# Optimization experiments

Measured on AMD Instinct MI355X. Metric: run time of the kernel, lower is better.

## Reference

```python
import jax, jax.numpy as jnp
import numpy as np

V, D, NH, L, T, B = 32000, 768, 12, 4, 2048, 1
HD = D // NH
THETA = 10000.0
EPS = 1e-5


def setup_inputs() -> dict:
    key = jax.random.key(0)
    ks = jax.random.split(key, 12)
    s = 0.02
    return {
        "idx": jax.random.randint(ks[0], (B, T), 0, V),
        "wte": jax.random.normal(ks[1], (V, D), jnp.float32) * s,
        "ln1_w": jnp.ones((L, D), jnp.float32),
        "attn_w": jax.random.normal(ks[2], (L, 3 * D, D), jnp.float32) * s,
        "attnproj_w": jax.random.normal(ks[3], (L, D, D), jnp.float32) * s,
        "ln2_w": jnp.ones((L, D), jnp.float32),
        "fc_w": jax.random.normal(ks[4], (L, 4 * D, D), jnp.float32) * s,
        "fc_b": jnp.zeros((L, 4 * D), jnp.float32),
        "proj_w": jax.random.normal(ks[5], (L, D, 4 * D), jnp.float32) * s,
        "proj_b": jnp.zeros((L, D), jnp.float32),
        "lnf_w": jnp.ones((D,), jnp.float32),
        "unemb_b": jnp.zeros((V,), jnp.float32),
    }


def _ln(x, w):
    mu = jnp.mean(x, axis=-1, keepdims=True)
    var = jnp.mean(jnp.square(x - mu), axis=-1, keepdims=True)
    return (x - mu) * jax.lax.rsqrt(var + EPS) * w


def _rope(x, cos, sin):
    # x: [B,NH,T,HD]; cos/sin: [T,HD//2]
    x1, x2 = x[..., : HD // 2], x[..., HD // 2 :]
    return jnp.concatenate([x1 * cos - x2 * sin, x1 * sin + x2 * cos], axis=-1)


def _forward(idx, wte, ln1_w, attn_w, attnproj_w, ln2_w, fc_w, fc_b, proj_w, proj_b, lnf_w, unemb_b):
    x = wte[idx]  # [B,T,D]
    inv_freq = 1.0 / (THETA ** (jnp.arange(0, HD, 2, dtype=jnp.float32) / HD))  # [HD/2]
    t = jnp.arange(T, dtype=jnp.float32)
    freqs = jnp.outer(t, inv_freq)  # [T, HD/2]
    cos, sin = jnp.cos(freqs), jnp.sin(freqs)
    causal = jnp.tril(jnp.ones((T, T), bool))
    scale = 1.0 / jnp.sqrt(jnp.asarray(HD, x.dtype))
    for l in range(L):
        h = _ln(x, ln1_w[l])
        qkv = h @ attn_w[l].T  # [B,T,3D]
        q, k, v = jnp.split(qkv, 3, axis=-1)
        q = q.reshape(B, T, NH, HD).transpose(0, 2, 1, 3)
        k = k.reshape(B, T, NH, HD).transpose(0, 2, 1, 3)
        v = v.reshape(B, T, NH, HD).transpose(0, 2, 1, 3)
        q, k = _rope(q, cos, sin), _rope(k, cos, sin)
        att = jnp.einsum("bhqd,bhkd->bhqk", q, k) * scale
        att = jnp.where(causal, att, -jnp.inf)
        att = jax.nn.softmax(att, axis=-1)
        y = jnp.einsum("bhqk,bhkd->bhqd", att, v)
        y = y.transpose(0, 2, 1, 3).reshape(B, T, D)
        x = x + y @ attnproj_w[l].T
        h = _ln(x, ln2_w[l])
        m = jax.nn.gelu(h @ fc_w[l].T + fc_b[l], approximate=False)
        x = x + m @ proj_w[l].T + proj_b[l]
    x = _ln(x, lnf_w)
    return x @ wte.T + unemb_b  # tied unembedding, [B,T,V]


def reference(idx, wte, ln1_w, attn_w, attnproj_w, ln2_w, fc_w, fc_b, proj_w, proj_b, lnf_w, unemb_b):
    return _forward(idx, wte, ln1_w, attn_w, attnproj_w, ln2_w, fc_w, fc_b, proj_w, proj_b, lnf_w, unemb_b)
```

## Files before the change

### kernel.cpp

```cpp
#include <hip/hip_runtime.h>
#include <hip/hip_bf16.h>

typedef __bf16 bf16_t;
typedef __bf16 bf16x8 __attribute__((ext_vector_type(8)));
typedef __bf16 bf16x4 __attribute__((ext_vector_type(4)));
typedef float  f32x4  __attribute__((ext_vector_type(4)));

__device__ __forceinline__ void gl_lds16(const void* g, void* l) {
    __builtin_amdgcn_global_load_lds(
        (__attribute__((address_space(1))) void*)g,
        (__attribute__((address_space(3))) void*)l, 16, 0, 0);
}

template <int N>
__device__ __forceinline__ void wait_vm() {
    if constexpr (N == 0)      asm volatile("s_waitcnt vmcnt(0)" ::: "memory");
    else if constexpr (N == 3) asm volatile("s_waitcnt vmcnt(3)" ::: "memory");
    else                       asm volatile("s_waitcnt vmcnt(4)" ::: "memory");
}

__global__ void cvt_kernel(const float* __restrict__ in, bf16_t* __restrict__ out,
                           int n4) {
    const int i = blockIdx.x * 256 + threadIdx.x;
    if (i < n4) {
        const float4 v = ((const float4*)in)[i];
        bf16x4 o;
        o.x = (bf16_t)v.x; o.y = (bf16_t)v.y; o.z = (bf16_t)v.z; o.w = (bf16_t)v.w;
        ((bf16x4*)out)[i] = o;
    }
}

__global__ void cvt4_kernel(const float* __restrict__ s0, const float* __restrict__ s1,
                            const float* __restrict__ s2, const float* __restrict__ s3,
                            bf16_t* __restrict__ d0, bf16_t* __restrict__ d1,
                            bf16_t* __restrict__ d2, bf16_t* __restrict__ d3,
                            int n0, int n1, int n2, int n3) {
    int j = blockIdx.x * 256 + threadIdx.x;
    const float* s; bf16_t* d;
    if (j < n0) { s = s0; d = d0; }
    else {
        j -= n0;
        if (j < n1) { s = s1; d = d1; }
        else {
            j -= n1;
            if (j < n2) { s = s2; d = d2; }
            else {
                j -= n2;
                if (j >= n3) return;
                s = s3; d = d3;
            }
        }
    }
    const float4 v = ((const float4*)s)[j];
    bf16x4 o;
    o.x = (bf16_t)v.x; o.y = (bf16_t)v.y; o.z = (bf16_t)v.z; o.w = (bf16_t)v.w;
    ((bf16x4*)d)[j] = o;
}

__global__ void rope_table(float* __restrict__ tab) {
    const int i = blockIdx.x * 256 + threadIdx.x;
    const int t = i >> 5, f = i & 31;
    const float inv_freq = __powf(10000.0f, -(float)f * (1.0f / 32.0f));
    const float ang = (float)t * inv_freq;
    float s, c;
    __sincosf(ang, &s, &c);
    tab[2 * i]     = c;
    tab[2 * i + 1] = s;
}

__global__ void embed_kernel(const int* __restrict__ idx,
                             const float* __restrict__ wte,
                             float* __restrict__ x) {
    const int t = blockIdx.x;
    const int row = idx[t];
    const float4* w = (const float4*)(wte + (size_t)row * 768);
    float4* o = (float4*)(x + (size_t)t * 768);
    if (threadIdx.x < 192) o[threadIdx.x] = w[threadIdx.x];
}

__global__ __launch_bounds__(256) void ln_kernel(const float* __restrict__ x,
                                                 const float* __restrict__ w,
                                                 bf16_t* __restrict__ out) {
    const int t = blockIdx.x, tid = threadIdx.x;
    __shared__ float red[256];
    const float* xr = x + (size_t)t * 768;
    const float v0 = xr[tid], v1 = xr[tid + 256], v2 = xr[tid + 512];
    red[tid] = v0 + v1 + v2;
    __syncthreads();
    for (int s = 128; s > 0; s >>= 1) {
        if (tid < s) red[tid] += red[tid + s];
        __syncthreads();
    }
    const float mu = red[0] * (1.0f / 768.0f);
    __syncthreads();
    const float d0 = v0 - mu, d1 = v1 - mu, d2 = v2 - mu;
    red[tid] = d0 * d0 + d1 * d1 + d2 * d2;
    __syncthreads();
    for (int s = 128; s > 0; s >>= 1) {
        if (tid < s) red[tid] += red[tid + s];
        __syncthreads();
    }
    const float rstd = rsqrtf(red[0] * (1.0f / 768.0f) + 1e-5f);
    bf16_t* orow = out + (size_t)t * 768;
    orow[tid]       = (bf16_t)(d0 * rstd * w[tid]);
    orow[tid + 256] = (bf16_t)(d1 * rstd * w[tid + 256]);
    orow[tid + 512] = (bf16_t)(d2 * rstd * w[tid + 512]);
}

__global__ __launch_bounds__(256) void rope_prep(const float* __restrict__ qkv,
                                                 const float* __restrict__ tab,
                                                 bf16_t* __restrict__ Qb,
                                                 bf16_t* __restrict__ Kb,
                                                 bf16_t* __restrict__ Vt) {
    const int t0 = blockIdx.x * 64, h = blockIdx.y;
    const int tid = threadIdx.x;
    __shared__ bf16_t vt[64][65];

    #pragma unroll
    for (int it = 0; it < 16; ++it) {
        const int item = it * 256 + tid;
        const int tl = item >> 6;
        const int which = (item >> 5) & 1;
        const int i = item & 31;
        const float* src = qkv + (size_t)(t0 + tl) * 2304 + which * 768 + h * 64;
        const float2 cs = ((const float2*)tab)[(t0 + tl) * 32 + i];
        const float c = cs.x, s = cs.y;
        const float x1 = src[i], x2 = src[i + 32];
        bf16_t* dst = (which ? Kb : Qb) + ((size_t)h * 2048 + t0 + tl) * 64;
        const float sc = which ? 1.0f : 0.125f;
        dst[i]      = (bf16_t)((x1 * c - x2 * s) * sc);
        dst[i + 32] = (bf16_t)((x1 * s + x2 * c) * sc);
    }

    #pragma unroll
    for (int pass = 0; pass < 4; ++pass) {
        const int r = pass * 16 + (tid >> 4);
        const int c = (tid & 15) * 4;
        const float4 v = *(const float4*)(qkv + (size_t)(t0 + r) * 2304 + 1536 + h * 64 + c);
        vt[c + 0][r] = (bf16_t)v.x;
        vt[c + 1][r] = (bf16_t)v.y;
        vt[c + 2][r] = (bf16_t)v.z;
        vt[c + 3][r] = (bf16_t)v.w;
    }
    __syncthreads();
    #pragma unroll
    for (int pass = 0; pass < 2; ++pass) {
        const int d = pass * 32 + (tid >> 3);
        const int k8 = (tid & 7) * 8;
        bf16x8 vv;
        #pragma unroll
        for (int j = 0; j < 8; ++j) vv[j] = vt[d][k8 + j];
        *(bf16x8*)(Vt + ((size_t)h * 64 + d) * 2048 + t0 + k8) = vv;
    }
}

__global__ __launch_bounds__(256) void attn_mfma(const bf16_t* __restrict__ Qb,
                                                 const bf16_t* __restrict__ Kb,
                                                 const bf16_t* __restrict__ Vt,
                                                 bf16_t* __restrict__ y) {
    const int qt = (int)gridDim.x - 1 - (int)blockIdx.x;
    const int h  = blockIdx.y;
    const int q0 = qt * 64;
    const int tid = threadIdx.x;
    const int w = tid >> 6, lane = tid & 63;
    const int lg = lane >> 4;
    const int ll = lane & 15;

    __shared__ bf16_t Ks[64 * 64];
    __shared__ bf16_t Vs[64 * 64];
    __shared__ bf16_t Ps[64 * 64];

    bf16x8 aq0, aq1;
    {
        const bf16_t* qp = Qb + ((size_t)h * 2048 + q0 + w * 16 + ll) * 64 + lg * 8;
        aq0 = *(const bf16x8*)qp;
        aq1 = *(const bf16x8*)(qp + 32);
    }

    f32x4 o[4];
    #pragma unroll
    for (int i = 0; i < 4; ++i) o[i] = (f32x4)(0.0f);
    float m_i[4], l_i[4];
    #pragma unroll
    for (int r = 0; r < 4; ++r) { m_i[r] = -3e38f; l_i[r] = 0.0f; }

    const int srow0 = tid >> 3;
    const int srow1 = srow0 + 32;
    const int sc16  = tid & 7;

    const bf16_t* Kbase = Kb + (size_t)h * 2048 * 64;
    const bf16_t* Vbase = Vt + (size_t)h * 64 * 2048;

    for (int kt = 0; kt <= qt; ++kt) {
        __syncthreads();
        {
            const bf16_t* kg = Kbase + (size_t)(kt * 64) * 64;
            const bf16x8 k0 = *(const bf16x8*)(kg + srow0 * 64 + sc16 * 8);
            const bf16x8 k1 = *(const bf16x8*)(kg + srow1 * 64 + sc16 * 8);
            const bf16_t* vg = Vbase + kt * 64;
            const bf16x8 v0 = *(const bf16x8*)(vg + (size_t)srow0 * 2048 + sc16 * 8);
            const bf16x8 v1 = *(const bf16x8*)(vg + (size_t)srow1 * 2048 + sc16 * 8);
            *(bf16x8*)((char*)(Ks + srow0 * 64) + ((sc16 * 16) ^ ((srow0 & 7) << 4))) = k0;
            *(bf16x8*)((char*)(Ks + srow1 * 64) + ((sc16 * 16) ^ ((srow1 & 7) << 4))) = k1;
            *(bf16x8*)((char*)(Vs + srow0 * 64) + ((sc16 * 16) ^ ((srow0 & 7) << 4))) = v0;
            *(bf16x8*)((char*)(Vs + srow1 * 64) + ((sc16 * 16) ^ ((srow1 & 7) << 4))) = v1;
        }
        __syncthreads();

        f32x4 sacc[4];
        #pragma unroll
        for (int kb = 0; kb < 4; ++kb) {
            const int krow = kb * 16 + ll;
            const char* kr = (const char*)(Ks + krow * 64);
            const int sw = (krow & 7) << 4;
            const bf16x8 b0 = *(const bf16x8*)(kr + ((lg * 16) ^ sw));
            const bf16x8 b1 = *(const bf16x8*)(kr + ((64 + lg * 16) ^ sw));
            sacc[kb] = __builtin_amdgcn_mfma_f32_16x16x32_bf16(aq0, b0, (f32x4)(0.0f), 0, 0, 0);
            sacc[kb] = __builtin_amdgcn_mfma_f32_16x16x32_bf16(aq1, b1, sacc[kb], 0, 0, 0);
        }

        float sc_[4][4];
        const bool diag = (kt == qt);
        #pragma unroll
        for (int kb = 0; kb < 4; ++kb) {
            #pragma unroll
            for (int r = 0; r < 4; ++r) {
                float v = sacc[kb][r];
                if (diag && (kb * 16 + ll) > (w * 16 + lg * 4 + r)) v = -3e38f;
                sc_[kb][r] = v;
            }
        }
        float rmax[4];
        #pragma unroll
        for (int r = 0; r < 4; ++r)
            rmax[r] = fmaxf(fmaxf(sc_[0][r], sc_[1][r]), fmaxf(sc_[2][r], sc_[3][r]));
        #pragma unroll
        for (int st = 0; st < 4; ++st) {
            const int off = 1 << st;
            #pragma unroll
            for (int r = 0; r < 4; ++r)
                rmax[r] = fmaxf(rmax[r], __shfl_xor(rmax[r], off));
        }
        float alpha[4], rsum[4];
        #pragma unroll
        for (int r = 0; r < 4; ++r) {
            const float mn = fmaxf(m_i[r], rmax[r]);
            alpha[r] = __expf(m_i[r] - mn);
            m_i[r] = mn;
            rsum[r] = 0.0f;
        }
        #pragma unroll
        for (int kb = 0; kb < 4; ++kb) {
            #pragma unroll
            for (int r = 0; r < 4; ++r) {
                const float p = __expf(sc_[kb][r] - m_i[r]);
                sc_[kb][r] = p;
                rsum[r] += p;
            }
        }
        #pragma unroll
        for (int st = 0; st < 4; ++st) {
            const int off = 1 << st;
            #pragma unroll
            for (int r = 0; r < 4; ++r)
                rsum[r] += __shfl_xor(rsum[r], off);
        }
        #pragma unroll
        for (int r = 0; r < 4; ++r) l_i[r] = l_i[r] * alpha[r] + rsum[r];

        #pragma unroll
        for (int r = 0; r < 4; ++r) {
            const int prow = w * 16 + lg * 4 + r;
            char* pb = (char*)(Ps + prow * 64);
            const int sw = (prow & 7) << 4;
            #pragma unroll
            for (int kb = 0; kb < 4; ++kb)
                *(bf16_t*)(pb + (((kb * 16 + ll) * 2) ^ sw)) = (bf16_t)sc_[kb][r];
        }

        #pragma unroll
        for (int db = 0; db < 4; ++db)
            #pragma unroll
            for (int r = 0; r < 4; ++r) o[db][r] *= alpha[r];

        #pragma unroll
        for (int ks = 0; ks < 2; ++ks) {
            const int arow = w * 16 + ll;
            const bf16x8 ap = *(const bf16x8*)((const char*)(Ps + arow * 64) +
                                ((ks * 64 + lg * 16) ^ ((arow & 7) << 4)));
            #pragma unroll
            for (int db = 0; db < 4; ++db) {
                const int vrow = db * 16 + ll;
                const bf16x8 bv = *(const bf16x8*)((const char*)(Vs + vrow * 64) +
                                    ((ks * 64 + lg * 16) ^ ((vrow & 7) << 4)));
                o[db] = __builtin_amdgcn_mfma_f32_16x16x32_bf16(ap, bv, o[db], 0, 0, 0);
            }
        }
    }

    #pragma unroll
    for (int r = 0; r < 4; ++r) {
        const float inv = 1.0f / l_i[r];
        bf16_t* yo = y + (size_t)(q0 + w * 16 + lg * 4 + r) * 768 + h * 64 + ll;
        #pragma unroll
        for (int db = 0; db < 4; ++db)
            yo[db * 16] = (bf16_t)(o[db][r] * inv);
    }
}

template <int FLAGS, int BM>
__global__ __launch_bounds__(256) void gemm_bt(const bf16_t* __restrict__ A,
                                               const bf16_t* __restrict__ B,
                                               const float* __restrict__ bias,
                                               float* __restrict__ C32,
                                               bf16_t* __restrict__ Cb,
                                               int M, int N, int K) {
    constexpr bool HAS_BIAS = (FLAGS & 1) != 0;
    constexpr bool HAS_RES  = (FLAGS & 2) != 0;
    constexpr bool HAS_GELU = (FLAGS & 4) != 0;
    constexpr bool OUT_BF16 = (FLAGS & 8) != 0;
    constexpr bool UNEMB    = (FLAGS & 16) != 0;
    constexpr int  WM       = (BM == 128) ? 64 : 32;
    constexpr int  MI       = WM / 16;
    constexpr int  NLOADS   = (BM == 128) ? 4 : 3;

    __shared__ bf16_t smem[2 * (BM + 128) * 32];
    bf16_t* As0 = smem;
    bf16_t* Bs0 = As0 + BM * 32;
    bf16_t* As1 = Bs0 + 128 * 32;
    bf16_t* Bs1 = As1 + BM * 32;

    const int tid = threadIdx.x;
    const int w = tid >> 6, lane = tid & 63;

    int bm, bn;
    if constexpr (UNEMB) {
        const int bid  = (int)blockIdx.y * (int)gridDim.x + (int)blockIdx.x;
        const int per  = ((int)gridDim.x * (int)gridDim.y) >> 3;
        const int nid  = (bid & 7) * per + (bid >> 3);
        bm = (nid & 15) * BM;
        bn = (nid >> 4) * 128;
    } else {
        bm = blockIdx.y * BM;
        bn = blockIdx.x * 128;
    }
    const int wm = (w >> 1) * WM, wn = (w & 1) * 64;

    const int sc = (lane & 3) * 8;
    const int srB = w * 32 + (lane >> 2);
    const bf16_t* gB0 = B + (size_t)(bn + srB) * K + sc;
    const bf16_t* gB1 = gB0 + (size_t)16 * K;
    const int srA = (BM == 128) ? srB : (w * 16 + (lane >> 2));
    const bf16_t* gA0 = A + (size_t)(bm + srA) * K + sc;
    const bf16_t* gA1 = gA0 + (size_t)16 * K;
    const int ldsA = ((BM == 128) ? (w * 32) : (w * 16)) * 32;
    const int ldsB = (w * 32) * 32;

    const int mrow  = lane & 15;
    const int khalf = (lane >> 4) * 8;

    f32x4 acc[MI][4];
    #pragma unroll
    for (int i = 0; i < MI; ++i)
        #pragma unroll
        for (int j = 0; j < 4; ++j) acc[i][j] = (f32x4)(0.0f);

    auto stage = [&](bf16_t* Ap, bf16_t* Bp, int kk) {
        gl_lds16(gA0 + kk, Ap + ldsA);
        if constexpr (BM == 128) gl_lds16(gA1 + kk, Ap + ldsA + 16 * 32);
        gl_lds16(gB0 + kk, Bp + ldsB);
        gl_lds16(gB1 + kk, Bp + ldsB + 16 * 32);
    };
    auto compute = [&](const bf16_t* Ap, const bf16_t* Bp) {
        bf16x8 af[MI], bfr[4];
        #pragma unroll
        for (int i = 0; i < MI; ++i)
            af[i] = *(const bf16x8*)(Ap + (wm + i * 16 + mrow) * 32 + khalf);
        #pragma unroll
        for (int j = 0; j < 4; ++j)
            bfr[j] = *(const bf16x8*)(Bp + (wn + j * 16 + mrow) * 32 + khalf);
        #pragma unroll
        for (int i = 0; i < MI; ++i)
            #pragma unroll
            for (int j = 0; j < 4; ++j)
                acc[i][j] = __builtin_amdgcn_mfma_f32_16x16x32_bf16(
                    af[i], bfr[j], acc[i][j], 0, 0, 0);
    };

    stage(As0, Bs0, 0);
    for (int k0 = 0; k0 < K; k0 += 64) {
        stage(As1, Bs1, k0 + 32);
        wait_vm<NLOADS>();
        __builtin_amdgcn_s_barrier();
        __builtin_amdgcn_sched_barrier(0);
        compute(As0, Bs0);
        __builtin_amdgcn_sched_barrier(0);
        __builtin_amdgcn_s_barrier();
        const bool more = (k0 + 64) < K;
        if (more) stage(As0, Bs0, k0 + 64);
        if (more) wait_vm<NLOADS>(); else wait_vm<0>();
        __builtin_amdgcn_s_barrier();
        __builtin_amdgcn_sched_barrier(0);
        compute(As1, Bs1);
        __builtin_amdgcn_sched_barrier(0);
        __builtin_amdgcn_s_barrier();
    }

    const int ccol = lane & 15;
    const int crow = (lane >> 4) * 4;
    #pragma unroll
    for (int i = 0; i < MI; ++i) {
        #pragma unroll
        for (int j = 0; j < 4; ++j) {
            const int col = bn + wn + j * 16 + ccol;
            #pragma unroll
            for (int r = 0; r < 4; ++r) {
                const int row = bm + wm + i * 16 + crow + r;
                float v = acc[i][j][r];
                if constexpr (HAS_BIAS) v += bias[col];
                if constexpr (HAS_GELU) v = 0.5f * v * (1.0f + erff(v * 0.70710678f));
                const size_t off = (size_t)row * N + col;
                if constexpr (HAS_RES) v += C32[off];
                if constexpr (OUT_BF16) Cb[off] = (bf16_t)v;
                else C32[off] = v;
            }
        }
    }
}

extern "C" void kernel_launch(void* const* d_in, const int* in_sizes, int n_in,
                              void* d_out, int out_size, void* d_ws, size_t ws_size,
                              hipStream_t stream) {
    const int T = 2048, D = 768, NH = 12, L = 4, V = 32000;
    const int D3 = 3 * D, D4 = 4 * D;

    const int*   idx        = (const int*)d_in[0];
    const float* wte        = (const float*)d_in[1];
    const float* ln1_w      = (const float*)d_in[2];
    const float* attn_w     = (const float*)d_in[3];
    const float* attnproj_w = (const float*)d_in[4];
    const float* ln2_w      = (const float*)d_in[5];
    const float* fc_w       = (const float*)d_in[6];
    const float* fc_b       = (const float*)d_in[7];
    const float* proj_w     = (const float*)d_in[8];
    const float* proj_b     = (const float*)d_in[9];
    const float* lnf_w      = (const float*)d_in[10];
    const float* unemb_b    = (const float*)d_in[11];
    float* out = (float*)d_out;

    char* p = (char*)d_ws;
    float*  X      = (float*)p;   p += (size_t)T * D * 4;
    bf16_t* Hb     = (bf16_t*)p;  p += (size_t)T * D * 2;
    float*  QKV    = (float*)p;
    bf16_t* Mb     = (bf16_t*)p;  p += (size_t)T * D3 * 4;
    bf16_t* wte_b  = (bf16_t*)p;  p += (size_t)V * D * 2;
    bf16_t* w_attn = (bf16_t*)p;  p += (size_t)D3 * D * 2;
    bf16_t* w_apr  = (bf16_t*)p;  p += (size_t)D * D * 2;
    bf16_t* w_fc   = (bf16_t*)p;  p += (size_t)D4 * D * 2;
    bf16_t* w_proj = (bf16_t*)p;  p += (size_t)D * D4 * 2;
    float*  rtab   = (float*)p;   p += (size_t)T * 32 * 2 * 4;

    bf16_t* Qb  = wte_b;
    bf16_t* Kbf = Qb  + (size_t)NH * T * 64;
    bf16_t* Vtg = Kbf + (size_t)NH * T * 64;

    embed_kernel<<<T, 256, 0, stream>>>(idx, wte, X);
    rope_table<<<T * 32 / 256, 256, 0, stream>>>(rtab);

    const int na = D3 * D / 4, nb = D * D / 4, nc = D4 * D / 4, nd = D * D4 / 4;
    const int ntot = na + nb + nc + nd;

    for (int l = 0; l < L; ++l) {
        cvt4_kernel<<<(ntot + 255) / 256, 256, 0, stream>>>(
            attn_w + (size_t)l * D3 * D, attnproj_w + (size_t)l * D * D,
            fc_w + (size_t)l * D4 * D, proj_w + (size_t)l * D * D4,
            w_attn, w_apr, w_fc, w_proj, na, nb, nc, nd);

        ln_kernel<<<T, 256, 0, stream>>>(X, ln1_w + (size_t)l * D, Hb);
        gemm_bt<0, 128><<<dim3(D3 / 128, T / 128), 256, 0, stream>>>(
            Hb, w_attn, nullptr, QKV, nullptr, T, D3, D);
        rope_prep<<<dim3(T / 64, NH), 256, 0, stream>>>(QKV, rtab, Qb, Kbf, Vtg);
        attn_mfma<<<dim3(T / 64, NH), 256, 0, stream>>>(Qb, Kbf, Vtg, Hb);
        gemm_bt<2, 64><<<dim3(D / 128, T / 64), 256, 0, stream>>>(
            Hb, w_apr, nullptr, X, nullptr, T, D, D);
        ln_kernel<<<T, 256, 0, stream>>>(X, ln2_w + (size_t)l * D, Hb);
        gemm_bt<13, 128><<<dim3(D4 / 128, T / 128), 256, 0, stream>>>(
            Hb, w_fc, fc_b + (size_t)l * D4, nullptr, Mb, T, D4, D);
        gemm_bt<3, 64><<<dim3(D / 128, T / 64), 256, 0, stream>>>(
            Mb, w_proj, proj_b + (size_t)l * D, X, nullptr, T, D, D4);
    }

    ln_kernel<<<T, 256, 0, stream>>>(X, lnf_w, Hb);
    {
        const int n4 = V * D / 4;
        cvt_kernel<<<(n4 + 255) / 256, 256, 0, stream>>>(wte, wte_b, n4);
    }
    gemm_bt<17, 128><<<dim3(T / 128, V / 128), 256, 0, stream>>>(
        Hb, wte_b, unemb_b, out, nullptr, T, V, D);
}
```

Baseline: 1.289 ms.

## Emit bf16 QKV, prefetch K/V in attention, batch weight conversion, widen unembedding tile

The QKV GEMM now writes bf16 instead of fp32, and rope_prep reads bf16 with wider vector loads. This halves QKV traffic but rounds pre-RoPE values to bf16. Attention register-prefetches the next K/V tile while the current one is being computed, to overlap global loads with MFMA work. All layer weights are converted to bf16 in one launch before the layer loop instead of once per layer, which needs more workspace. The unembedding GEMM uses a 128x256 tile with 512 threads to improve reuse on the largest GEMM.

Result: faster. 1.232 ms (-4.4%).

```diff
diff --git a/kernel.cpp b/kernel.cpp
--- a/kernel.cpp
+++ b/kernel.cpp
@@ -107,7 +107,7 @@
     orow[tid + 512] = (bf16_t)(d2 * rstd * w[tid + 512]);
 }
 
-__global__ __launch_bounds__(256) void rope_prep(const float* __restrict__ qkv,
+__global__ __launch_bounds__(256) void rope_prep(const bf16_t* __restrict__ qkv,
                                                  const float* __restrict__ tab,
                                                  bf16_t* __restrict__ Qb,
                                                  bf16_t* __restrict__ Kb,
@@ -122,10 +122,10 @@
         const int tl = item >> 6;
         const int which = (item >> 5) & 1;
         const int i = item & 31;
-        const float* src = qkv + (size_t)(t0 + tl) * 2304 + which * 768 + h * 64;
+        const bf16_t* src = qkv + (size_t)(t0 + tl) * 2304 + which * 768 + h * 64;
         const float2 cs = ((const float2*)tab)[(t0 + tl) * 32 + i];
         const float c = cs.x, s = cs.y;
-        const float x1 = src[i], x2 = src[i + 32];
+        const float x1 = (float)src[i], x2 = (float)src[i + 32];
         bf16_t* dst = (which ? Kb : Qb) + ((size_t)h * 2048 + t0 + tl) * 64;
         const float sc = which ? 1.0f : 0.125f;
         dst[i]      = (bf16_t)((x1 * c - x2 * s) * sc);
@@ -133,14 +133,12 @@
     }
 
     #pragma unroll
-    for (int pass = 0; pass < 4; ++pass) {
-        const int r = pass * 16 + (tid >> 4);
-        const int c = (tid & 15) * 4;
-        const float4 v = *(const float4*)(qkv + (size_t)(t0 + r) * 2304 + 1536 + h * 64 + c);
-        vt[c + 0][r] = (bf16_t)v.x;
-        vt[c + 1][r] = (bf16_t)v.y;
-        vt[c + 2][r] = (bf16_t)v.z;
-        vt[c + 3][r] = (bf16_t)v.w;
+    for (int pass = 0; pass < 2; ++pass) {
+        const int r = pass * 32 + (tid >> 3);
+        const int c = (tid & 7) * 8;
+        const bf16x8 v = *(const bf16x8*)(qkv + (size_t)(t0 + r) * 2304 + 1536 + h * 64 + c);
+        #pragma unroll
+        for (int j = 0; j < 8; ++j) vt[c + j][r] = v[j];
     }
     __syncthreads();
     #pragma unroll
@@ -191,21 +189,31 @@
     const bf16_t* Kbase = Kb + (size_t)h * 2048 * 64;
     const bf16_t* Vbase = Vt + (size_t)h * 64 * 2048;
 
+    bf16x8 pk0, pk1, pv0, pv1;
+    {
+        const bf16_t* kg = Kbase;
+        pk0 = *(const bf16x8*)(kg + srow0 * 64 + sc16 * 8);
+        pk1 = *(const bf16x8*)(kg + srow1 * 64 + sc16 * 8);
+        pv0 = *(const bf16x8*)(Vbase + (size_t)srow0 * 2048 + sc16 * 8);
+        pv1 = *(const bf16x8*)(Vbase + (size_t)srow1 * 2048 + sc16 * 8);
+    }
+
     for (int kt = 0; kt <= qt; ++kt) {
         __syncthreads();
-        {
-            const bf16_t* kg = Kbase + (size_t)(kt * 64) * 64;
-            const bf16x8 k0 = *(const bf16x8*)(kg + srow0 * 64 + sc16 * 8);
-            const bf16x8 k1 = *(const bf16x8*)(kg + srow1 * 64 + sc16 * 8);
-            const bf16_t* vg = Vbase + kt * 64;
-            const bf16x8 v0 = *(const bf16x8*)(vg + (size_t)srow0 * 2048 + sc16 * 8);
-            const bf16x8 v1 = *(const bf16x8*)(vg + (size_t)srow1 * 2048 + sc16 * 8);
-            *(bf16x8*)((char*)(Ks + srow0 * 64) + ((sc16 * 16) ^ ((srow0 & 7) << 4))) = k0;
-            *(bf16x8*)((char*)(Ks + srow1 * 64) + ((sc16 * 16) ^ ((srow1 & 7) << 4))) = k1;
-            *(bf16x8*)((char*)(Vs + srow0 * 64) + ((sc16 * 16) ^ ((srow0 & 7) << 4))) = v0;
-            *(bf16x8*)((char*)(Vs + srow1 * 64) + ((sc16 * 16) ^ ((srow1 & 7) << 4))) = v1;
-        }
+        *(bf16x8*)((char*)(Ks + srow0 * 64) + ((sc16 * 16) ^ ((srow0 & 7) << 4))) = pk0;
+        *(bf16x8*)((char*)(Ks + srow1 * 64) + ((sc16 * 16) ^ ((srow1 & 7) << 4))) = pk1;
+        *(bf16x8*)((char*)(Vs + srow0 * 64) + ((sc16 * 16) ^ ((srow0 & 7) << 4))) = pv0;
+        *(bf16x8*)((char*)(Vs + srow1 * 64) + ((sc16 * 16) ^ ((srow1 & 7) << 4))) = pv1;
         __syncthreads();
+
+        if (kt < qt) {
+            const bf16_t* kg = Kbase + (size_t)((kt + 1) * 64) * 64;
+            pk0 = *(const bf16x8*)(kg + srow0 * 64 + sc16 * 8);
+            pk1 = *(const bf16x8*)(kg + srow1 * 64 + sc16 * 8);
+            const bf16_t* vg = Vbase + (kt + 1) * 64;
+            pv0 = *(const bf16x8*)(vg + (size_t)srow0 * 2048 + sc16 * 8);
+            pv1 = *(const bf16x8*)(vg + (size_t)srow1 * 2048 + sc16 * 8);
+        }
 
         f32x4 sacc[4];
         #pragma unroll
@@ -308,26 +316,28 @@
     }
 }
 
-template <int FLAGS, int BM>
-__global__ __launch_bounds__(256) void gemm_bt(const bf16_t* __restrict__ A,
-                                               const bf16_t* __restrict__ B,
-                                               const float* __restrict__ bias,
-                                               float* __restrict__ C32,
-                                               bf16_t* __restrict__ Cb,
-                                               int M, int N, int K) {
+template <int FLAGS, int BM, int BN>
+__global__ __launch_bounds__((BN == 256) ? 512 : 256)
+void gemm_bt(const bf16_t* __restrict__ A,
+             const bf16_t* __restrict__ B,
+             const float* __restrict__ bias,
+             float* __restrict__ C32,
+             bf16_t* __restrict__ Cb,
+             int M, int N, int K) {
     constexpr bool HAS_BIAS = (FLAGS & 1) != 0;
     constexpr bool HAS_RES  = (FLAGS & 2) != 0;
     constexpr bool HAS_GELU = (FLAGS & 4) != 0;
     constexpr bool OUT_BF16 = (FLAGS & 8) != 0;
     constexpr bool UNEMB    = (FLAGS & 16) != 0;
-    constexpr int  WM       = (BM == 128) ? 64 : 32;
+    constexpr bool WIDE     = (BN == 256);
+    constexpr int  WM       = WIDE ? 64 : ((BM == 128) ? 64 : 32);
     constexpr int  MI       = WM / 16;
-    constexpr int  NLOADS   = (BM == 128) ? 4 : 3;
-
-    __shared__ bf16_t smem[2 * (BM + 128) * 32];
+    constexpr int  NLOADS   = WIDE ? 3 : ((BM == 128) ? 4 : 3);
+
+    __shared__ bf16_t smem[2 * (BM + BN) * 32];
     bf16_t* As0 = smem;
     bf16_t* Bs0 = As0 + BM * 32;
-    bf16_t* As1 = Bs0 + 128 * 32;
+    bf16_t* As1 = Bs0 + BN * 32;
     bf16_t* Bs1 = As1 + BM * 32;
 
     const int tid = threadIdx.x;
@@ -339,22 +349,24 @@
         const int per  = ((int)gridDim.x * (int)gridDim.y) >> 3;
         const int nid  = (bid & 7) * per + (bid >> 3);
         bm = (nid & 15) * BM;
-        bn = (nid >> 4) * 128;
+        bn = (nid >> 4) * BN;
     } else {
         bm = blockIdx.y * BM;
-        bn = blockIdx.x * 128;
-    }
-    const int wm = (w >> 1) * WM, wn = (w & 1) * 64;
+        bn = blockIdx.x * BN;
+    }
+    int wm, wn;
+    if constexpr (WIDE) { wm = (w >> 2) * 64; wn = (w & 3) * 64; }
+    else                { wm = (w >> 1) * WM; wn = (w & 1) * 64; }
 
     const int sc = (lane & 3) * 8;
     const int srB = w * 32 + (lane >> 2);
     const bf16_t* gB0 = B + (size_t)(bn + srB) * K + sc;
     const bf16_t* gB1 = gB0 + (size_t)16 * K;
-    const int srA = (BM == 128) ? srB : (w * 16 + (lane >> 2));
+    const int ldsB = (w * 32) * 32;
+    const int srA = (!WIDE && BM == 128) ? srB : (w * 16 + (lane >> 2));
     const bf16_t* gA0 = A + (size_t)(bm + srA) * K + sc;
     const bf16_t* gA1 = gA0 + (size_t)16 * K;
-    const int ldsA = ((BM == 128) ? (w * 32) : (w * 16)) * 32;
-    const int ldsB = (w * 32) * 32;
+    const int ldsA = ((!WIDE && BM == 128) ? (w * 32) : (w * 16)) * 32;
 
     const int mrow  = lane & 15;
     const int khalf = (lane >> 4) * 8;
@@ -367,7 +379,7 @@
 
     auto stage = [&](bf16_t* Ap, bf16_t* Bp, int kk) {
         gl_lds16(gA0 + kk, Ap + ldsA);
-        if constexpr (BM == 128) gl_lds16(gA1 + kk, Ap + ldsA + 16 * 32);
+        if constexpr (!WIDE && BM == 128) gl_lds16(gA1 + kk, Ap + ldsA + 16 * 32);
         gl_lds16(gB0 + kk, Bp + ldsB);
         gl_lds16(gB1 + kk, Bp + ldsB + 16 * 32);
     };
@@ -451,13 +463,13 @@
     char* p = (char*)d_ws;
     float*  X      = (float*)p;   p += (size_t)T * D * 4;
     bf16_t* Hb     = (bf16_t*)p;  p += (size_t)T * D * 2;
-    float*  QKV    = (float*)p;
-    bf16_t* Mb     = (bf16_t*)p;  p += (size_t)T * D3 * 4;
+    bf16_t* QKVb   = (bf16_t*)p;
+    bf16_t* Mb     = QKVb;        p += (size_t)T * D4 * 2;
     bf16_t* wte_b  = (bf16_t*)p;  p += (size_t)V * D * 2;
-    bf16_t* w_attn = (bf16_t*)p;  p += (size_t)D3 * D * 2;
-    bf16_t* w_apr  = (bf16_t*)p;  p += (size_t)D * D * 2;
-    bf16_t* w_fc   = (bf16_t*)p;  p += (size_t)D4 * D * 2;
-    bf16_t* w_proj = (bf16_t*)p;  p += (size_t)D * D4 * 2;
+    bf16_t* w_attn = (bf16_t*)p;  p += (size_t)L * D3 * D * 2;
+    bf16_t* w_apr  = (bf16_t*)p;  p += (size_t)L * D * D * 2;
+    bf16_t* w_fc   = (bf16_t*)p;  p += (size_t)L * D4 * D * 2;
+    bf16_t* w_proj = (bf16_t*)p;  p += (size_t)L * D * D4 * 2;
     float*  rtab   = (float*)p;   p += (size_t)T * 32 * 2 * 4;
 
     bf16_t* Qb  = wte_b;
@@ -467,27 +479,26 @@
     embed_kernel<<<T, 256, 0, stream>>>(idx, wte, X);
     rope_table<<<T * 32 / 256, 256, 0, stream>>>(rtab);
 
-    const int na = D3 * D / 4, nb = D * D / 4, nc = D4 * D / 4, nd = D * D4 / 4;
+    const int na = L * D3 * D / 4, nb = L * D * D / 4;
+    const int nc = L * D4 * D / 4, nd = L * D * D4 / 4;
     const int ntot = na + nb + nc + nd;
+    cvt4_kernel<<<(ntot + 255) / 256, 256, 0, stream>>>(
+        attn_w, attnproj_w, fc_w, proj_w,
+        w_attn, w_apr, w_fc, w_proj, na, nb, nc, nd);
 
     for (int l = 0; l < L; ++l) {
-        cvt4_kernel<<<(ntot + 255) / 256, 256, 0, stream>>>(
-            attn_w + (size_t)l * D3 * D, attnproj_w + (size_t)l * D * D,
-            fc_w + (size_t)l * D4 * D, proj_w + (size_t)l * D * D4,
-            w_attn, w_apr, w_fc, w_proj, na, nb, nc, nd);
-
         ln_kernel<<<T, 256, 0, stream>>>(X, ln1_w + (size_t)l * D, Hb);
-        gemm_bt<0, 128><<<dim3(D3 / 128, T / 128), 256, 0, stream>>>(
-            Hb, w_attn, nullptr, QKV, nullptr, T, D3, D);
-        rope_prep<<<dim3(T / 64, NH), 256, 0, stream>>>(QKV, rtab, Qb, Kbf, Vtg);
+        gemm_bt<8, 128, 128><<<dim3(D3 / 128, T / 128), 256, 0, stream>>>(
+            Hb, w_attn + (size_t)l * D3 * D, nullptr, nullptr, QKVb, T, D3, D);
+        rope_prep<<<dim3(T / 64, NH), 256, 0, stream>>>(QKVb, rtab, Qb, Kbf, Vtg);
         attn_mfma<<<dim3(T / 64, NH), 256, 0, stream>>>(Qb, Kbf, Vtg, Hb);
-        gemm_bt<2, 64><<<dim3(D / 128, T / 64), 256, 0, stream>>>(
-            Hb, w_apr, nullptr, X, nullptr, T, D, D);
+        gemm_bt<2, 64, 128><<<dim3(D / 128, T / 64), 256, 0, stream>>>(
+            Hb, w_apr + (size_t)l * D * D, nullptr, X, nullptr, T, D, D);
         ln_kernel<<<T, 256, 0, stream>>>(X, ln2_w + (size_t)l * D, Hb);
-        gemm_bt<13, 128><<<dim3(D4 / 128, T / 128), 256, 0, stream>>>(
-            Hb, w_fc, fc_b + (size_t)l * D4, nullptr, Mb, T, D4, D);
-        gemm_bt<3, 64><<<dim3(D / 128, T / 64), 256, 0, stream>>>(
-            Mb, w_proj, proj_b + (size_t)l * D, X, nullptr, T, D, D4);
+        gemm_bt<13, 128, 128><<<dim3(D4 / 128, T / 128), 256, 0, stream>>>(
+            Hb, w_fc + (size_t)l * D4 * D, fc_b + (size_t)l * D4, nullptr, Mb, T, D4, D);
+        gemm_bt<3, 64, 128><<<dim3(D / 128, T / 64), 256, 0, stream>>>(
+            Mb, w_proj + (size_t)l * D * D4, proj_b + (size_t)l * D, X, nullptr, T, D, D4);
     }
 
     ln_kernel<<<T, 256, 0, stream>>>(X, lnf_w, Hb);
@@ -495,6 +506,6 @@
         const int n4 = V * D / 4;
         cvt_kernel<<<(n4 + 255) / 256, 256, 0, stream>>>(wte, wte_b, n4);
     }
-    gemm_bt<17, 128><<<dim3(T / 128, V / 128), 256, 0, stream>>>(
+    gemm_bt<17, 128, 256><<<dim3(T / 128, V / 256), 512, 0, stream>>>(
         Hb, wte_b, unemb_b, out, nullptr, T, V, D);
 }
```
